# Performance work log

Measured on AMD Instinct MI355X. Metric: run time of the kernel, lower is better.

## Reference

```python
import jax, jax.numpy as jnp
import numpy as np

K = 3  # kernel_size


def setup_inputs() -> dict:
    key = jax.random.key(0)
    k1, k2, k3, k4, k5 = jax.random.split(key, 5)
    B, H, W, C, F = 8, 128, 128, 64, 128
    x_in = jax.random.normal(k1, (B, H, W, C), dtype=jnp.float32)
    # offset-predicting conv: k x k conv, C -> k*k channels (small init so offsets are moderate)
    offset_W = jax.random.normal(k2, (K, K, C, K * K), dtype=jnp.float32) * 0.05
    offset_b = jax.random.normal(k3, (K * K,), dtype=jnp.float32) * 0.05
    # main deformable conv weights: (k, k, C_in, F)
    conv_W = jax.random.normal(k4, (K, K, C, F), dtype=jnp.float32) * (1.0 / np.sqrt(K * K * C))
    conv_b = jax.random.normal(k5, (F,), dtype=jnp.float32) * 0.01
    return {"x_in": x_in, "offset_W": offset_W, "offset_b": offset_b,
            "conv_W": conv_W, "conv_b": conv_b}


def reference(x_in, offset_W, offset_b, conv_W, conv_b):
    B, H, W, C = x_in.shape
    k = offset_W.shape[0]
    pad = k // 2
    # 1) predict one scalar offset per output location per kernel tap
    offsets = jax.lax.conv_general_dilated(
        x_in, offset_W, window_strides=(1, 1), padding='SAME',
        dimension_numbers=('NHWC', 'HWIO', 'NHWC')) + offset_b  # (B,H,W,k*k)
    offsets = offsets.reshape(B, H, W, k, k)

    # 2) sampling grid: integer rows (clamped), fractional cols = base + offset
    i = jnp.arange(H)
    j = jnp.arange(W)
    p = jnp.arange(k) - pad
    q = jnp.arange(k) - pad
    yy = jnp.clip(i[:, None, None, None] + p[None, None, :, None], 0, H - 1)  # (H,1,k,1)
    yy = jnp.broadcast_to(yy, (H, W, k, k))
    xf = (j[None, :, None, None] + q[None, None, None, :]).astype(x_in.dtype) + offsets  # (B,H,W,k,k)
    x0 = jnp.floor(xf)
    w1 = xf - x0                                   # linear-interp weight, grads flow to offsets
    x0i = jnp.clip(x0.astype(jnp.int32), 0, W - 1)
    x1i = jnp.clip(x0i + 1, 0, W - 1)

    # 3) bilinear (1-D linear) gather per batch element
    def sample(xb, x0b, x1b, wb):
        s0 = xb[yy, x0b]  # (H,W,k,k,C)
        s1 = xb[yy, x1b]
        return s0 * (1.0 - wb[..., None]) + s1 * wb[..., None]

    sampled = jax.vmap(sample)(x_in, x0i, x1i, w1)  # (B,H,W,k,k,C)

    # 4) weighted convolution sum over taps and input channels
    out = jnp.einsum('bijpqc,pqcf->bijf', sampled, conv_W) + conv_b  # (B,H,W,F)
    return out
```

## Files before the change

### kernel.cpp

```cpp
#include <hip/hip_runtime.h>
#include <hip/hip_bf16.h>


typedef __attribute__((ext_vector_type(8))) short short8;
typedef __attribute__((ext_vector_type(4))) float f32x4;

#define CWB_BYTES  (18 * 4 * 128 * 8 * 2)
#define OWT_OFF    CWB_BYTES
#define OWT_BYTES  (9 * 9 * 64 * 4)
#define OFFS_OFF   (OWT_OFF + OWT_BYTES)
#define OFFS_BYTES (131072 * 9 * 4)
#define WS_SPLIT   (OFFS_OFF + OFFS_BYTES)

__device__ __forceinline__ unsigned short f2bf(float f) {
  union { float f; unsigned u; } v; v.f = f;
  unsigned r = v.u + 0x7fffu + ((v.u >> 16) & 1u);
  return (unsigned short)(r >> 16);
}

__device__ __forceinline__ unsigned pk2bf(float a, float b) {
  __hip_bfloat162 h = __float22bfloat162_rn(make_float2(a, b));
  union { __hip_bfloat162 h; unsigned u; } c; c.h = h;
  return c.u;
}

__global__ __launch_bounds__(256) void pack_kernel(
    const float* __restrict__ cW, const float* __restrict__ oW,
    unsigned short* __restrict__ cWb, float* __restrict__ oWt) {
  const int t = blockIdx.x * 256 + threadIdx.x;
  if (t < 73728) {
    const int k = t >> 7, f = t & 127;
    const int ks = k >> 5, q4 = (k >> 3) & 3, jj = k & 7;
    cWb[(size_t)(((ks * 4 + q4) * 128 + f) * 8 + jj)] = f2bf(cW[t]);
  }
  if (t < 5184) {
    const int pq = t / 576;
    const int r = t - pq * 576;
    const int tt = r >> 6;
    const int ch = r & 63;
    oWt[t] = oW[(size_t)(pq * 64 + ch) * 9 + tt];
  }
}

__global__ __launch_bounds__(256) void offsets_kernel(
    const float* __restrict__ x, const float* __restrict__ oWt,
    const float* __restrict__ ob, float* __restrict__ offs) {
  __shared__ __align__(16) float wL[81 * 64];
  const int tid = threadIdx.x;
  for (int it = tid; it < 1296; it += 256)
    ((float4*)wL)[it] = ((const float4*)oWt)[it];
  __syncthreads();

  const int hw = blockIdx.x;
  const int logical = ((hw & 7) << 10) | (hw >> 3);
  const int gpix = logical * 16 + (tid >> 4);
  const int c4 = tid & 15;
  const int j = gpix & 127;
  const int i = (gpix >> 7) & 127;
  const int b = gpix >> 14;
  const float* xb = x + ((size_t)b << 20);

  float acc[9];
#pragma unroll
  for (int t = 0; t < 9; ++t) acc[t] = 0.f;

#pragma unroll
  for (int p = 0; p < 3; ++p) {
    const int yy = i + p - 1;
    if (yy < 0 || yy > 127) continue;
#pragma unroll
    for (int q = 0; q < 3; ++q) {
      const int xx = j + q - 1;
      if (xx < 0 || xx > 127) continue;
      const float4 v = ((const float4*)(xb + (((yy << 7) + xx) << 6)))[c4];
      const float4* wrow = (const float4*)wL + (p * 3 + q) * 9 * 16 + c4;
#pragma unroll
      for (int t = 0; t < 9; ++t) {
        const float4 w4 = wrow[t * 16];
        acc[t] += v.x * w4.x + v.y * w4.y + v.z * w4.z + v.w * w4.w;
      }
    }
  }
#pragma unroll
  for (int t = 0; t < 9; ++t) {
    acc[t] += __shfl_xor(acc[t], 1);
    acc[t] += __shfl_xor(acc[t], 2);
    acc[t] += __shfl_xor(acc[t], 4);
    acc[t] += __shfl_xor(acc[t], 8);
  }
  if (c4 == 0) {
    float* op = offs + (size_t)gpix * 9;
#pragma unroll
    for (int t = 0; t < 9; ++t) op[t] = acc[t] + ob[t];
  }
}

__global__ __launch_bounds__(512, 2) void main_kernel(
    const float* __restrict__ x, const float* __restrict__ offs,
    const float* __restrict__ cb, float* __restrict__ out,
    const unsigned short* __restrict__ cWb) {
  __shared__ __align__(16) char lds[64 * 576 * 2];
  __shared__ float offw[576];
  __shared__ int gpk[576];

  const int tid = threadIdx.x;
  const int hwbid = blockIdx.x;
  const int bid = ((hwbid & 7) << 8) | (hwbid >> 3);
  const int j0 = (bid & 1) << 6;
  const int i = (bid >> 1) & 127;
  const int b = bid >> 8;
  const float* xb = x + ((size_t)b << 20);

  const int lane = tid & 63;
  const int wv = tid >> 6;

  const size_t base9 = ((size_t)(((b << 7) | i) << 7) | j0) * 9;
  for (int item = tid; item < 576; item += 512) {
    const int pix = item / 9;
    const int tap = item - pix * 9;
    const float off = offs[base9 + item];
    const int p = tap / 3;
    const int q = tap - p * 3;
    int yy = i + p - 1;
    yy = yy < 0 ? 0 : (yy > 127 ? 127 : yy);
    const float xf = (float)(j0 + pix + q - 1) + off;
    const float x0f = floorf(xf);
    const float w1 = xf - x0f;
    int x0i = (int)x0f;
    x0i = x0i < 0 ? 0 : (x0i > 127 ? 127 : x0i);
    const int x1i = (x0i + 1 > 127) ? 127 : x0i + 1;
    gpk[item] = ((((yy << 7) + x0i) << 8)) | (x1i - x0i);
    offw[item] = w1;
  }
  __syncthreads();

#pragma unroll
  for (int batch = 0; batch < 6; ++batch) {
    int a0_[3], a1_[3], sb[3];
    float sw1[3];
#pragma unroll
    for (int s = 0; s < 3; ++s) {
      const int idx = tid + (batch * 3 + s) * 512;
      const int c4 = idx & 15;
      const int pair = idx >> 4;
      const int g = gpk[pair];
      sw1[s] = offw[pair];
      const int base = g & ~255;
      a0_[s] = base + (c4 << 4);
      a1_[s] = a0_[s] + ((g & 1) << 8);
      const int pix8 = (pair / 9) & 7;
      sb[s] = ((pair << 7) + (c4 << 3)) ^ (pix8 << 4);
    }
    float4 s0[3], s1[3];
#pragma unroll
    for (int s = 0; s < 3; ++s) {
      s0[s] = *(const float4*)((const char*)xb + a0_[s]);
      s1[s] = *(const float4*)((const char*)xb + a1_[s]);
    }
    asm volatile("" :: "v"(s0[0].x), "v"(s0[1].x), "v"(s0[2].x),
                       "v"(s1[0].x), "v"(s1[1].x), "v"(s1[2].x));
    __builtin_amdgcn_sched_barrier(0);
#pragma unroll
    for (int s = 0; s < 3; ++s) {
      const float w1 = sw1[s];
      uint2 pk;
      pk.x = pk2bf(s0[s].x + w1 * (s1[s].x - s0[s].x),
                   s0[s].y + w1 * (s1[s].y - s0[s].y));
      pk.y = pk2bf(s0[s].z + w1 * (s1[s].z - s0[s].z),
                   s0[s].w + w1 * (s1[s].w - s0[s].w));
      *(uint2*)(lds + sb[s]) = pk;
    }
  }
  __syncthreads();

  const int f0 = wv << 4;
  const int colf = lane & 15;
  const int q4 = lane >> 4;
  f32x4 a0 = {0.f, 0.f, 0.f, 0.f}, a1 = a0, a2 = a0, a3 = a0;
  short8 bf;
  {
    const unsigned short* wb = cWb + (size_t)((q4 * 128 + f0 + colf) * 8);
    bf = *(const short8*)wb;
  }
  for (int ks = 0; ks < 18; ++ks) {
    const int aoff = (colf * 1152 + ks * 64 + q4 * 16) ^ ((colf & 7) << 4);
    const short8 af0 = *(const short8*)(lds + aoff);
    const short8 af1 = *(const short8*)(lds + aoff + 16 * 1152);
    const short8 af2 = *(const short8*)(lds + aoff + 32 * 1152);
    const short8 af3 = *(const short8*)(lds + aoff + 48 * 1152);
    short8 nb;
    if (ks < 17) {
      nb = *(const short8*)(cWb +
            (size_t)((((ks + 1) * 4 + q4) * 128 + f0 + colf) * 8));
    }
    a0 = __builtin_amdgcn_mfma_f32_16x16x32_bf16(bf, af0, a0, 0, 0, 0);
    a1 = __builtin_amdgcn_mfma_f32_16x16x32_bf16(bf, af1, a1, 0, 0, 0);
    a2 = __builtin_amdgcn_mfma_f32_16x16x32_bf16(bf, af2, a2, 0, 0, 0);
    a3 = __builtin_amdgcn_mfma_f32_16x16x32_bf16(bf, af3, a3, 0, 0, 0);
    if (ks < 17) bf = nb;
  }
  __syncthreads();

  float* const outS = (float*)lds;
  {
    const float4 cbv = *(const float4*)(cb + f0 + q4 * 4);
    float4 r;
    r.x = a0[0] + cbv.x; r.y = a0[1] + cbv.y;
    r.z = a0[2] + cbv.z; r.w = a0[3] + cbv.w;
    *(float4*)(outS + (colf) * 132 + f0 + q4 * 4) = r;
    r.x = a1[0] + cbv.x; r.y = a1[1] + cbv.y;
    r.z = a1[2] + cbv.z; r.w = a1[3] + cbv.w;
    *(float4*)(outS + (16 + colf) * 132 + f0 + q4 * 4) = r;
    r.x = a2[0] + cbv.x; r.y = a2[1] + cbv.y;
    r.z = a2[2] + cbv.z; r.w = a2[3] + cbv.w;
    *(float4*)(outS + (32 + colf) * 132 + f0 + q4 * 4) = r;
    r.x = a3[0] + cbv.x; r.y = a3[1] + cbv.y;
    r.z = a3[2] + cbv.z; r.w = a3[3] + cbv.w;
    *(float4*)(outS + (48 + colf) * 132 + f0 + q4 * 4) = r;
  }
  __syncthreads();
  float4* og = (float4*)(out + (((size_t)((b << 14) | (i << 7) | j0)) << 7));
#pragma unroll
  for (int r = 0; r < 4; ++r) {
    const int f4i = r * 512 + tid;
    const int pp = f4i >> 5, ff = f4i & 31;
    og[pp * 32 + ff] = *(const float4*)(outS + pp * 132 + ff * 4);
  }
}

__global__ __launch_bounds__(512, 8) void fused_deform_kernel(
    const float* __restrict__ x, const float* __restrict__ oW,
    const float* __restrict__ ob, const float* __restrict__ cW,
    const float* __restrict__ cb, float* __restrict__ out) {
  __shared__ __align__(16) char lds[32 * 576 * 2];
  __shared__ float offs_s[288];
  float* const xtile = (float*)lds;

  const int tid = threadIdx.x;
  const int bid = blockIdx.x;
  const int j0 = (bid & 3) << 5;
  const int i = (bid >> 2) & 127;
  const int b = bid >> 9;
  const float* xb = x + ((size_t)b << 20);
  const int lane = tid & 63;
  const int wv = tid >> 6;

  for (int t = tid; t < 3 * 34 * 16; t += 512) {
    const int c4 = t & 15;
    const int cc = (t >> 4) % 34;
    const int r = (t >> 4) / 34;
    const int row = i + r - 1;
    const int col = j0 + cc - 1;
    float4 v = make_float4(0.f, 0.f, 0.f, 0.f);
    if (row >= 0 && row <= 127 && col >= 0 && col <= 127)
      v = ((const float4*)(xb + (((row << 7) + col) << 6)))[c4];
    *(float4*)(xtile + (r * 34 + cc) * 68 + c4 * 4) = v;
  }
  __syncthreads();

  for (int t = tid; t < 576; t += 512) {
    const int half = t & 1;
    const int item = t >> 1;
    const int ochan = item % 9;
    const int pix = item / 9;
    const int c4base = half << 3;
    f32x4 acc = {0.f, 0.f, 0.f, 0.f};
#pragma unroll
    for (int pq = 0; pq < 9; ++pq) {
      const int p = pq / 3, q = pq - p * 3;
      const float4* xr = (const float4*)(xtile + (p * 34 + pix + q) * 68) + c4base;
      const float* wr = oW + (size_t)(pq * 64 + c4base * 4) * 9 + ochan;
#pragma unroll
      for (int c4 = 0; c4 < 8; ++c4) {
        const float4 v = xr[c4];
        acc.x += v.x * wr[(c4 * 4 + 0) * 9];
        acc.y += v.y * wr[(c4 * 4 + 1) * 9];
        acc.z += v.z * wr[(c4 * 4 + 2) * 9];
        acc.w += v.w * wr[(c4 * 4 + 3) * 9];
      }
    }
    float s = (acc.x + acc.y) + (acc.z + acc.w);
    s += __shfl_xor(s, 1);
    if (!half) offs_s[item] = s + ob[ochan];
  }
  __syncthreads();

  for (int it = tid; it < 32 * 9 * 16; it += 512) {
    const int c4 = it & 15;
    const int tmp = it >> 4;
    const int tap = tmp % 9;
    const int pix = tmp / 9;
    const int j = j0 + pix;
    const float off = offs_s[pix * 9 + tap];
    const int p = tap / 3;
    const int q = tap - p * 3;
    int yy = i + p - 1;
    yy = yy < 0 ? 0 : (yy > 127 ? 127 : yy);
    const float xf = (float)(j + q - 1) + off;
    const float x0f = floorf(xf);
    const float w1 = xf - x0f;
    int x0i = (int)x0f;
    x0i = x0i < 0 ? 0 : (x0i > 127 ? 127 : x0i);
    const int x1i = (x0i + 1 > 127) ? 127 : x0i + 1;
    const float4 s0 = ((const float4*)(xb + (((yy << 7) + x0i) << 6)))[c4];
    const float4 s1 = ((const float4*)(xb + (((yy << 7) + x1i) << 6)))[c4];
    const float w0 = 1.0f - w1;
    const int boff = (pix * 1152 + tap * 128 + c4 * 8) ^ ((pix & 7) << 4);
    uint2 pk;
    pk.x = (unsigned)f2bf(s0.x * w0 + s1.x * w1) |
           ((unsigned)f2bf(s0.y * w0 + s1.y * w1) << 16);
    pk.y = (unsigned)f2bf(s0.z * w0 + s1.z * w1) |
           ((unsigned)f2bf(s0.w * w0 + s1.w * w1) << 16);
    *(uint2*)(lds + boff) = pk;
  }
  __syncthreads();

  const int m = wv & 1;
  const int f0 = (wv >> 1) << 5;
  const int colf = lane & 15;
  const int q4 = lane >> 4;
  const int pixr = m * 16 + colf;
  f32x4 a0 = {0.f, 0.f, 0.f, 0.f}, a1 = a0;
  for (int ks = 0; ks < 18; ++ks) {
    const int aoff = (pixr * 1152 + ks * 64 + q4 * 16) ^ ((pixr & 7) << 4);
    const short8 af = *(const short8*)(lds + aoff);
    short8 bf0, bf1;
    const float* wp = cW + (size_t)(ks * 32 + q4 * 8) * 128 + f0 + colf;
#pragma unroll
    for (int jj = 0; jj < 8; ++jj) bf0[jj] = (short)f2bf(wp[jj * 128]);
#pragma unroll
    for (int jj = 0; jj < 8; ++jj) bf1[jj] = (short)f2bf(wp[jj * 128 + 16]);
    a0 = __builtin_amdgcn_mfma_f32_16x16x32_bf16(bf0, af, a0, 0, 0, 0);
    a1 = __builtin_amdgcn_mfma_f32_16x16x32_bf16(bf1, af, a1, 0, 0, 0);
  }

  const float cb0s = cb[f0 + colf];
  const float cb1s = cb[f0 + 16 + colf];
  float* obase = out + (((size_t)((b << 14) | (i << 7) | j0)) << 7);
#pragma unroll
  for (int reg = 0; reg < 4; ++reg) {
    float* r = obase + (size_t)(m * 16 + q4 * 4 + reg) * 128;
    r[f0 + colf] = a0[reg] + cb0s;
    r[f0 + 16 + colf] = a1[reg] + cb1s;
  }
}

extern "C" void kernel_launch(void* const* d_in, const int* in_sizes, int n_in,
                              void* d_out, int out_size, void* d_ws, size_t ws_size,
                              hipStream_t stream) {
  const float* x = (const float*)d_in[0];
  const float* oW = (const float*)d_in[1];
  const float* ob = (const float*)d_in[2];
  const float* cW = (const float*)d_in[3];
  const float* cb = (const float*)d_in[4];
  float* out = (float*)d_out;

  if (ws_size >= WS_SPLIT) {
    unsigned short* cWb = (unsigned short*)d_ws;
    float* oWt = (float*)((char*)d_ws + OWT_OFF);
    float* offs = (float*)((char*)d_ws + OFFS_OFF);
    hipLaunchKernelGGL(pack_kernel, dim3(288), dim3(256), 0, stream,
                       cW, oW, cWb, oWt);
    hipLaunchKernelGGL(offsets_kernel, dim3(8192), dim3(256), 0, stream,
                       x, oWt, ob, offs);
    hipLaunchKernelGGL(main_kernel, dim3(2048), dim3(512), 0, stream,
                       x, offs, cb, out, cWb);
  } else {
    hipLaunchKernelGGL(fused_deform_kernel, dim3(4096), dim3(512), 0, stream,
                       x, oW, ob, cW, cb, out);
  }
}
```

Before: 93.29 us.

## Fuse offset-prediction conv into main deformable kernel via LDS halo tile

Removes the separate offsets kernel and its global offset buffer, computing the 3x3 offset conv inside the main kernel from a 3x66x64 input halo staged in shared memory, with offsets kept in LDS. This cuts one kernel launch plus the global write and read of the offset tensor. In exchange each block does extra halo loads and offset FLOPs before the main gather, which adds serialized prologue work and increases LDS usage (73.7KB plus extras), and that may affect occupancy at 2 blocks per CU.

```diff
diff --git a/kernel.cpp b/kernel.cpp
--- a/kernel.cpp
+++ b/kernel.cpp
@@ -8,9 +8,11 @@
 #define CWB_BYTES  (18 * 4 * 128 * 8 * 2)
 #define OWT_OFF    CWB_BYTES
 #define OWT_BYTES  (9 * 9 * 64 * 4)
-#define OFFS_OFF   (OWT_OFF + OWT_BYTES)
-#define OFFS_BYTES (131072 * 9 * 4)
-#define WS_SPLIT   (OFFS_OFF + OFFS_BYTES)
+#define WS_NEED    (OWT_OFF + OWT_BYTES)
+
+#define WL_OFF    0
+#define HALO_OFF  20736
+#define OFFS_S_OFF 71424
 
 __device__ __forceinline__ unsigned short f2bf(float f) {
   union { float f; unsigned u; } v; v.f = f;
@@ -42,66 +44,17 @@
   }
 }
 
-__global__ __launch_bounds__(256) void offsets_kernel(
+__global__ __launch_bounds__(512, 2) void fused_kernel(
     const float* __restrict__ x, const float* __restrict__ oWt,
-    const float* __restrict__ ob, float* __restrict__ offs) {
-  __shared__ __align__(16) float wL[81 * 64];
-  const int tid = threadIdx.x;
-  for (int it = tid; it < 1296; it += 256)
-    ((float4*)wL)[it] = ((const float4*)oWt)[it];
-  __syncthreads();
-
-  const int hw = blockIdx.x;
-  const int logical = ((hw & 7) << 10) | (hw >> 3);
-  const int gpix = logical * 16 + (tid >> 4);
-  const int c4 = tid & 15;
-  const int j = gpix & 127;
-  const int i = (gpix >> 7) & 127;
-  const int b = gpix >> 14;
-  const float* xb = x + ((size_t)b << 20);
-
-  float acc[9];
-#pragma unroll
-  for (int t = 0; t < 9; ++t) acc[t] = 0.f;
-
-#pragma unroll
-  for (int p = 0; p < 3; ++p) {
-    const int yy = i + p - 1;
-    if (yy < 0 || yy > 127) continue;
-#pragma unroll
-    for (int q = 0; q < 3; ++q) {
-      const int xx = j + q - 1;
-      if (xx < 0 || xx > 127) continue;
-      const float4 v = ((const float4*)(xb + (((yy << 7) + xx) << 6)))[c4];
-      const float4* wrow = (const float4*)wL + (p * 3 + q) * 9 * 16 + c4;
-#pragma unroll
-      for (int t = 0; t < 9; ++t) {
-        const float4 w4 = wrow[t * 16];
-        acc[t] += v.x * w4.x + v.y * w4.y + v.z * w4.z + v.w * w4.w;
-      }
-    }
-  }
-#pragma unroll
-  for (int t = 0; t < 9; ++t) {
-    acc[t] += __shfl_xor(acc[t], 1);
-    acc[t] += __shfl_xor(acc[t], 2);
-    acc[t] += __shfl_xor(acc[t], 4);
-    acc[t] += __shfl_xor(acc[t], 8);
-  }
-  if (c4 == 0) {
-    float* op = offs + (size_t)gpix * 9;
-#pragma unroll
-    for (int t = 0; t < 9; ++t) op[t] = acc[t] + ob[t];
-  }
-}
-
-__global__ __launch_bounds__(512, 2) void main_kernel(
-    const float* __restrict__ x, const float* __restrict__ offs,
-    const float* __restrict__ cb, float* __restrict__ out,
-    const unsigned short* __restrict__ cWb) {
-  __shared__ __align__(16) char lds[64 * 576 * 2];
+    const float* __restrict__ ob, const float* __restrict__ cb,
+    float* __restrict__ out, const unsigned short* __restrict__ cWb) {
+  __shared__ __align__(16) char lds[73728];
   __shared__ float offw[576];
   __shared__ int gpk[576];
+
+  float* const wL = (float*)(lds + WL_OFF);
+  float* const halo = (float*)(lds + HALO_OFF);
+  float* const offs_s = (float*)(lds + OFFS_S_OFF);
 
   const int tid = threadIdx.x;
   const int hwbid = blockIdx.x;
@@ -114,11 +67,59 @@
   const int lane = tid & 63;
   const int wv = tid >> 6;
 
-  const size_t base9 = ((size_t)(((b << 7) | i) << 7) | j0) * 9;
+  for (int it = tid; it < 1296; it += 512)
+    ((float4*)wL)[it] = ((const float4*)oWt)[it];
+  for (int it = tid; it < 3 * 66 * 16; it += 512) {
+    const int c4 = it & 15;
+    const int hr = it >> 4;
+    const int cc = hr % 66;
+    const int r = hr / 66;
+    const int grow = i + r - 1;
+    const int gcol = j0 + cc - 1;
+    float4 v = make_float4(0.f, 0.f, 0.f, 0.f);
+    if (grow >= 0 && grow <= 127 && gcol >= 0 && gcol <= 127)
+      v = ((const float4*)(xb + (((grow << 7) + gcol) << 6)))[c4];
+    ((float4*)halo)[it] = v;
+  }
+  __syncthreads();
+
+#pragma unroll
+  for (int half = 0; half < 2; ++half) {
+    const int item = tid + half * 512;
+    const int pix = item >> 4;
+    const int c4 = item & 15;
+    float acc[9];
+#pragma unroll
+    for (int t = 0; t < 9; ++t) acc[t] = 0.f;
+#pragma unroll
+    for (int pq = 0; pq < 9; ++pq) {
+      const int p = pq / 3, q = pq - p * 3;
+      const float4 v = ((const float4*)(halo + ((p * 66 + pix + q) << 6)))[c4];
+      const float4* wrow = (const float4*)wL + pq * 9 * 16 + c4;
+#pragma unroll
+      for (int t = 0; t < 9; ++t) {
+        const float4 w4 = wrow[t * 16];
+        acc[t] += v.x * w4.x + v.y * w4.y + v.z * w4.z + v.w * w4.w;
+      }
+    }
+#pragma unroll
+    for (int t = 0; t < 9; ++t) {
+      acc[t] += __shfl_xor(acc[t], 1);
+      acc[t] += __shfl_xor(acc[t], 2);
+      acc[t] += __shfl_xor(acc[t], 4);
+      acc[t] += __shfl_xor(acc[t], 8);
+    }
+    if (c4 == 0) {
+#pragma unroll
+      for (int t = 0; t < 9; ++t) offs_s[pix * 9 + t] = acc[t] + ob[t];
+    }
+  }
+  __syncthreads();
+
   for (int item = tid; item < 576; item += 512) {
     const int pix = item / 9;
     const int tap = item - pix * 9;
-    const float off = offs[base9 + item];
+    const float off = offs_s[item];
     const int p = tap / 3;
     const int q = tap - p * 3;
     int yy = i + p - 1;
@@ -355,16 +356,13 @@
   const float* cb = (const float*)d_in[4];
   float* out = (float*)d_out;
 
-  if (ws_size >= WS_SPLIT) {
+  if (ws_size >= WS_NEED) {
     unsigned short* cWb = (unsigned short*)d_ws;
     float* oWt = (float*)((char*)d_ws + OWT_OFF);
-    float* offs = (float*)((char*)d_ws + OFFS_OFF);
     hipLaunchKernelGGL(pack_kernel, dim3(288), dim3(256), 0, stream,
                        cW, oW, cWb, oWt);
-    hipLaunchKernelGGL(offsets_kernel, dim3(8192), dim3(256), 0, stream,
-                       x, oWt, ob, offs);
-    hipLaunchKernelGGL(main_kernel, dim3(2048), dim3(512), 0, stream,
-                       x, offs, cb, out, cWb);
+    hipLaunchKernelGGL(fused_kernel, dim3(2048), dim3(512), 0, stream,
+                       x, oWt, ob, cb, out, cWb);
   } else {
     hipLaunchKernelGGL(fused_deform_kernel, dim3(4096), dim3(512), 0, stream,
                        x, oW, ob, cW, cb, out);
```

After: 90.70 us (median of 2 runs). 2.8% less time.
